# Performance work log

Measured on AMD Instinct MI355X. Metric: run time of the kernel, lower is better.

## Reference

```python
import jax, jax.numpy as jnp
import numpy as np

CONF_THRES = 0.25
IOU_THRES = 0.45
MAX_DET = 1000
MAX_WH = 4096.0  # class offset used by YOLOv5 for class-aware NMS
K = 1024         # fixed candidate count (static-shape stand-in for conf filtering)


def xywh2xyxy(b):
    cx, cy, w, h = b[..., 0], b[..., 1], b[..., 2], b[..., 3]
    return jnp.stack([cx - w / 2, cy - h / 2, cx + w / 2, cy + h / 2], axis=-1)


def pairwise_iou(boxes):
    # boxes: [K,4] xyxy -> [K,K] IoU
    x1, y1, x2, y2 = boxes[:, 0], boxes[:, 1], boxes[:, 2], boxes[:, 3]
    area = (x2 - x1) * (y2 - y1)
    ix1 = jnp.maximum(x1[:, None], x1[None, :])
    iy1 = jnp.maximum(y1[:, None], y1[None, :])
    ix2 = jnp.minimum(x2[:, None], x2[None, :])
    iy2 = jnp.minimum(y2[:, None], y2[None, :])
    inter = jnp.clip(ix2 - ix1, 0.0) * jnp.clip(iy2 - iy1, 0.0)
    return inter / (area[:, None] + area[None, :] - inter + 1e-9)


def nms_image(pred):
    # pred: [N, 5+nc] = xywh, obj, class scores
    boxes = xywh2xyxy(pred[:, :4])                 # [N,4]
    scores = pred[:, 5:] * pred[:, 4:5]            # conf = obj * cls
    conf = jnp.max(scores, axis=-1)                # [N]
    cls = jnp.argmax(scores, axis=-1)              # [N] int
    masked = jnp.where(conf > CONF_THRES, conf, -1.0)
    top_conf, idx = jax.lax.top_k(masked, K)       # sorted desc
    cand_boxes = boxes[idx]                        # [K,4]
    cand_cls = cls[idx]                            # [K]
    cand_valid = top_conf > 0.0                    # below-threshold slots are -1
    # class-aware NMS: offset boxes per class so different classes never overlap
    off_boxes = cand_boxes + (cand_cls.astype(pred.dtype) * MAX_WH)[:, None]
    iou = pairwise_iou(off_boxes)                  # [K,K]

    def step(suppressed, i):
        keep_i = jnp.logical_and(jnp.logical_not(suppressed[i]), cand_valid[i])
        suppressed = jnp.where(keep_i, jnp.logical_or(suppressed, iou[i] > IOU_THRES), suppressed)
        return suppressed, keep_i

    _, keep = jax.lax.scan(step, jnp.zeros((K,), dtype=bool), jnp.arange(K))
    sel_score = jnp.where(keep, top_conf, -1.0)
    fin_score, fin_idx = jax.lax.top_k(sel_score, MAX_DET)
    ok = fin_score > 0.0
    det = jnp.concatenate(
        [cand_boxes[fin_idx],
         top_conf[fin_idx][:, None],
         cand_cls[fin_idx].astype(pred.dtype)[:, None]],
        axis=-1,
    )  # [MAX_DET, 6] = x1,y1,x2,y2,conf,cls
    return jnp.where(ok[:, None], det, 0.0)


def setup_inputs() -> dict:
    key = jax.random.key(0)
    k1, k2, k3, k4 = jax.random.split(key, 4)
    B, N, NC = 16, 25200, 80
    cxcy = jax.random.uniform(k1, (B, N, 2), dtype=jnp.float32) * 640.0
    wh = jax.random.uniform(k2, (B, N, 2), dtype=jnp.float32) * 96.0 + 4.0
    obj = jax.random.uniform(k3, (B, N, 1), dtype=jnp.float32)
    cls = jax.random.uniform(k4, (B, N, NC), dtype=jnp.float32)
    pred = jnp.concatenate([cxcy, wh, obj, cls], axis=-1)
    return {"pred": pred}


def reference(pred):
    # [B, MAX_DET, 6] zero-padded detections per image
    return jax.vmap(nms_image)(pred)
```

## Files before the change

kernel.cpp:

```cpp
#include <hip/hip_runtime.h>
#include <stdint.h>

typedef unsigned int u32;
typedef unsigned long long u64;

#define BB 16
#define NN 25200
#define ROWLEN 85
#define KCAND 1024
#define MAXDET 1000
#define CONF_T 0.25f
#define IOU_T 0.45f
#define MAX_WH 4096.0f

__device__ __forceinline__ u32 f2key(float f) {
  u32 u = __float_as_uint(f);
  return (u & 0x80000000u) ? ~u : (u | 0x80000000u);
}
__device__ __forceinline__ float key2f(u32 k) {
  u32 u = (k & 0x80000000u) ? (k & 0x7FFFFFFFu) : ~k;
  return __uint_as_float(u);
}

__global__ __launch_bounds__(64) void k_score(const float* __restrict__ pred,
                                              float* __restrict__ masked,
                                              int* __restrict__ clsArr) {
  __shared__ float sh[64 * ROWLEN];
  const int t = threadIdx.x;
  const size_t blk = (size_t)blockIdx.x;
  const float4* src = (const float4*)(pred + blk * (64 * ROWLEN));
  float4* dst = (float4*)sh;
  #pragma unroll
  for (int i = 0; i < 21; ++i) dst[t + 64 * i] = src[t + 64 * i];
  if (t < 16) dst[t + 64 * 21] = src[t + 64 * 21];
  __syncthreads();
  const float* row = sh + t * ROWLEN;
  float obj = row[4];
  float v0 = -INFINITY, v1 = -INFINITY, v2 = -INFINITY, v3 = -INFINITY;
  int j0 = 0, j1 = 20, j2 = 40, j3 = 60;
  #pragma unroll
  for (int c = 0; c < 20; ++c) {
    float s0 = obj * row[5 + c];
    float s1 = obj * row[25 + c];
    float s2 = obj * row[45 + c];
    float s3 = obj * row[65 + c];
    if (s0 > v0) { v0 = s0; j0 = c; }
    if (s1 > v1) { v1 = s1; j1 = 20 + c; }
    if (s2 > v2) { v2 = s2; j2 = 40 + c; }
    if (s3 > v3) { v3 = s3; j3 = 60 + c; }
  }
  float v = v0; int j = j0;
  if (v1 > v) { v = v1; j = j1; }
  if (v2 > v) { v = v2; j = j2; }
  if (v3 > v) { v = v3; j = j3; }
  size_t r = blk * 64 + t;
  masked[r] = (v > CONF_T) ? v : -1.0f;
  clsArr[r] = j;
}

__device__ __forceinline__ void bt_apply(u64& e, u64 p, int m, int j, int k) {
  bool lower = ((m & j) == 0);
  bool dir = ((m & k) == 0);
  bool takeMax = (lower == dir);
  u64 mx = e > p ? e : p;
  u64 mn = e > p ? p : e;
  e = takeMax ? mx : mn;
}

__global__ __launch_bounds__(1024) void k_select(const float* __restrict__ pred,
                                                 const float* __restrict__ masked,
                                                 const int* __restrict__ clsArr,
                                                 float* __restrict__ candScore,
                                                 float* __restrict__ candBox,
                                                 int* __restrict__ candCls) {
  __shared__ u32 hist[16][257];
  __shared__ u64 buf[2048];
  __shared__ u32 sh_sel, sh_rem, sh_cnt;
  const int b = blockIdx.x;
  const int tid = threadIdx.x;
  const int lane = tid & 63;
  const int wv = tid >> 6;
  const float* m = masked + (size_t)b * NN;
  u32* histflat = (u32*)hist;

  u32 keys[25];
  #pragma unroll
  for (int it = 0; it < 25; ++it) {
    int n0 = tid + it * 1024;
    keys[it] = (n0 < NN) ? f2key(m[n0]) : 0u;
  }

  u32 prefix = 0, himask = 0, remaining = KCAND;
  for (int pass = 0; pass < 4; ++pass) {
    int shift = 24 - 8 * pass;
    for (int i = tid; i < 16 * 257; i += 1024) histflat[i] = 0;
    __syncthreads();
    #pragma unroll
    for (int it = 0; it < 25; ++it) {
      int n0 = tid + it * 1024;
      u32 key = keys[it];
      if (n0 < NN && (key & himask) == prefix)
        atomicAdd(&hist[wv][(key >> shift) & 255], 1u);
    }
    __syncthreads();
    if (wv == 0) {
      u32 c0 = 0, c1 = 0, c2 = 0, c3 = 0;
      #pragma unroll
      for (int w = 0; w < 16; ++w) {
        c0 += hist[w][4 * lane + 0];
        c1 += hist[w][4 * lane + 1];
        c2 += hist[w][4 * lane + 2];
        c3 += hist[w][4 * lane + 3];
      }
      u32 tl = c0 + c1 + c2 + c3;
      u32 incl = tl;
      #pragma unroll
      for (int off = 1; off <= 32; off <<= 1) {
        u32 o = __shfl_down(incl, off, 64);
        if (lane + off < 64) incl += o;
      }
      u32 S0 = incl;
      u32 S1 = S0 - c0;
      u32 S2 = S1 - c1;
      u32 S3 = S2 - c2;
      u32 S4 = S3 - c3;
      u32 rem = remaining;
      if (S0 >= rem && S1 < rem) { sh_sel = 4 * lane + 0; sh_rem = rem - S1; }
      if (S1 >= rem && S2 < rem) { sh_sel = 4 * lane + 1; sh_rem = rem - S2; }
      if (S2 >= rem && S3 < rem) { sh_sel = 4 * lane + 2; sh_rem = rem - S3; }
      if (S3 >= rem && S4 < rem) { sh_sel = 4 * lane + 3; sh_rem = rem - S4; }
    }
    __syncthreads();
    prefix |= (sh_sel << shift);
    remaining = sh_rem;
    himask |= (0xFFu << shift);
    __syncthreads();
  }
  const u32 T = prefix;
  if (tid == 0) sh_cnt = 0;
  __syncthreads();
  #pragma unroll
  for (int it = 0; it < 25; ++it) {
    int n0 = tid + it * 1024;
    u32 key = keys[it];
    bool match = (n0 < NN) && (key >= T);
    u64 bal = __ballot(match);
    if (bal) {
      int leader = __ffsll((unsigned long long)bal) - 1;
      u32 base = 0;
      u32 cnt = (u32)__popcll(bal);
      if (lane == leader) base = atomicAdd(&sh_cnt, cnt);
      base = __shfl(base, leader, 64);
      if (match) {
        u32 pos = base + (u32)__popcll(bal & ((1ull << lane) - 1ull));
        if (pos < 2048) buf[pos] = ((u64)key << 32) | (u32)(~(u32)n0);
      }
    }
  }
  __syncthreads();
  u32 c = sh_cnt; if (c > 2048) c = 2048;
  for (int t = tid; t < 2048; t += 1024) if (t >= (int)c) buf[t] = 0;
  __syncthreads();

  u64 e0 = buf[tid];
  u64 e1 = buf[tid + 1024];
  #pragma unroll
  for (int k = 2; k <= 64; k <<= 1) {
    #pragma unroll
    for (int j = k >> 1; j > 0; j >>= 1) {
      u64 p0 = __shfl_xor(e0, j, 64);
      u64 p1 = __shfl_xor(e1, j, 64);
      bt_apply(e0, p0, tid, j, k);
      bt_apply(e1, p1, tid + 1024, j, k);
    }
  }
  for (int k = 128; k <= 2048; k <<= 1) {
    int jstart = k >> 1;
    if (k == 2048) {
      u64 mx = e0 > e1 ? e0 : e1;
      u64 mn = e0 > e1 ? e1 : e0;
      e0 = mx; e1 = mn;
      jstart = 512;
    }
    for (int j = jstart; j >= 64; j >>= 1) {
      buf[tid] = e0; buf[tid + 1024] = e1;
      __syncthreads();
      u64 p0 = buf[tid ^ j];
      u64 p1 = buf[(tid ^ j) + 1024];
      bt_apply(e0, p0, tid, j, k);
      bt_apply(e1, p1, tid + 1024, j, k);
      __syncthreads();
    }
    #pragma unroll
    for (int j = 32; j > 0; j >>= 1) {
      u64 p0 = __shfl_xor(e0, j, 64);
      u64 p1 = __shfl_xor(e1, j, 64);
      bt_apply(e0, p0, tid, j, k);
      bt_apply(e1, p1, tid + 1024, j, k);
    }
  }
  {
    u64 e = e0;
    u32 key = (u32)(e >> 32);
    u32 idx = ~(u32)e;
    if (idx >= NN) idx = 0;
    float sc = key2f(key);
    size_t g = (size_t)b * KCAND + tid;
    candScore[g] = sc;
    const float* p = pred + ((size_t)b * NN + idx) * ROWLEN;
    float cx = p[0], cy = p[1], w = p[2], h = p[3];
    float4 bx;
    bx.x = cx - 0.5f * w;
    bx.y = cy - 0.5f * h;
    bx.z = cx + 0.5f * w;
    bx.w = cy + 0.5f * h;
    ((float4*)candBox)[g] = bx;
    candCls[g] = clsArr[(size_t)b * NN + idx];
  }
}

__global__ __launch_bounds__(256) void k_iou(const float* __restrict__ candBox,
                                             const int* __restrict__ candCls,
                                             u64* __restrict__ matT) {
  #pragma clang fp contract(off)
  __shared__ float sx1[KCAND], sy1[KCAND], sx2[KCAND], sy2[KCAND], sar[KCAND];
  const int b = blockIdx.y;
  const int r0 = blockIdx.x * 64;
  const int tid = threadIdx.x;
  for (int i = tid; i < KCAND; i += 256) {
    float4 bx = ((const float4*)candBox)[(size_t)b * KCAND + i];
    float off = (float)candCls[(size_t)b * KCAND + i] * MAX_WH;
    float x1 = bx.x + off, y1 = bx.y + off, x2 = bx.z + off, y2 = bx.w + off;
    sx1[i] = x1; sy1[i] = y1; sx2[i] = x2; sy2[i] = y2;
    sar[i] = (x2 - x1) * (y2 - y1);
  }
  __syncthreads();
  const int row = r0 + (tid & 63);
  const int wbase = tid >> 6;
  float rx1 = sx1[row], ry1 = sy1[row], rx2 = sx2[row], ry2 = sy2[row], rar = sar[row];
  for (int q = 0; q < 4; ++q) {
    int w = wbase + q * 4;
    int jb = w << 6;
    u64 mk = 0;
    for (int kk = 0; kk < 64; ++kk) {
      int jj = jb + kk;
      float ix1 = fmaxf(rx1, sx1[jj]);
      float iy1 = fmaxf(ry1, sy1[jj]);
      float ix2 = fminf(rx2, sx2[jj]);
      float iy2 = fminf(ry2, sy2[jj]);
      float dx = fmaxf(ix2 - ix1, 0.0f);
      float dy = fmaxf(iy2 - iy1, 0.0f);
      float inter = dx * dy;
      float den = rar + sar[jj];
      den = den - inter;
      den = den + 1e-9f;
      float iou = inter / den;
      if (iou > IOU_T) mk |= (1ull << kk);
    }
    matT[(((size_t)b * 16 + w) << 10) + row] = mk;
  }
}

__global__ __launch_bounds__(64, 1) void k_scan(const u64* __restrict__ matT,
                                                const float* __restrict__ candScore,
                                                u64* __restrict__ keepw) {
  const int b = blockIdx.x;
  const int lane = threadIdx.x;
  const u64* Mb = matT + ((size_t)b << 14);
  u64 vw[16];
  u64 dg16[16];
  #pragma unroll
  for (int w = 0; w < 16; ++w) {
    float sc = candScore[(size_t)b * KCAND + w * 64 + lane];
    vw[w] = __ballot(sc > 0.0f);
  }
  #pragma unroll
  for (int c = 0; c < 16; ++c)
    dg16[c] = Mb[((size_t)c << 10) + c * 64 + lane];

  u64 kcw[16];
  #pragma unroll
  for (int c = 0; c < 16; ++c) {
    u64 acc = 0;
    #pragma unroll
    for (int cp = 0; cp < c; ++cp) {
      u64 wv = Mb[((size_t)c << 10) + cp * 64 + lane];
      if ((kcw[cp] >> lane) & 1ull) acc |= wv;
    }
    #pragma unroll
    for (int st = 1; st < 64; st <<= 1) acc |= __shfl_xor(acc, st, 64);
    u64 d = dg16[c];
    u64 s = acc;
    u64 kc = 0;
    u64 vc = vw[c];
    #pragma unroll
    for (int g = 0; g < 8; ++g) {
      u64 dgp[8];
      #pragma unroll
      for (int j = 0; j < 8; ++j) dgp[j] = __shfl(d, g * 8 + j, 64);
      #pragma unroll
      for (int j = 0; j < 8; ++j) {
        int i = g * 8 + j;
        bool ok = !((s >> i) & 1ull) && ((vc >> i) & 1ull);
        if (ok) { s |= dgp[j]; kc |= (1ull << i); }
      }
    }
    kcw[c] = kc;
  }
  if (lane < 16) keepw[(size_t)b * 16 + lane] = kcw[lane];
}

__global__ __launch_bounds__(1024) void k_out(const u64* __restrict__ keepw,
                                              const float* __restrict__ candScore,
                                              const float* __restrict__ candBox,
                                              const int* __restrict__ candCls,
                                              float* __restrict__ out) {
  __shared__ u64 kw[16];
  const int b = blockIdx.x;
  const int tid = threadIdx.x;
  if (tid < 16) kw[tid] = keepw[(size_t)b * 16 + tid];
  __syncthreads();
  int total = 0;
  #pragma unroll
  for (int w = 0; w < 16; ++w) total += __popcll(kw[w]);
  int kept_eff = total < MAXDET ? total : MAXDET;
  const int t = tid;
  u64 word = kw[t >> 6];
  int bit = (int)((word >> (t & 63)) & 1ull);
  int rank = 0;
  for (int w = 0; w < (t >> 6); ++w) rank += __popcll(kw[w]);
  rank += __popcll(word & ((1ull << (t & 63)) - 1ull));
  float* outb = out + (size_t)b * MAXDET * 6;
  if (bit && rank < MAXDET) {
    size_t g = (size_t)b * KCAND + t;
    float4 bx = ((const float4*)candBox)[g];
    float sc = candScore[g];
    float cf = (float)candCls[g];
    float* o = outb + (size_t)rank * 6;
    o[0] = bx.x; o[1] = bx.y; o[2] = bx.z; o[3] = bx.w; o[4] = sc; o[5] = cf;
  }
  if (t < MAXDET && t >= kept_eff) {
    float* o = outb + (size_t)t * 6;
    o[0] = 0.f; o[1] = 0.f; o[2] = 0.f; o[3] = 0.f; o[4] = 0.f; o[5] = 0.f;
  }
}

extern "C" void kernel_launch(void* const* d_in, const int* in_sizes, int n_in,
                              void* d_out, int out_size, void* d_ws, size_t ws_size,
                              hipStream_t stream) {
  const float* pred = (const float*)d_in[0];
  float* out = (float*)d_out;
  char* ws = (char*)d_ws;
  size_t o = 0;
  float* masked    = (float*)(ws + o); o += (size_t)BB * NN * 4;
  int*   clsArr    = (int*)  (ws + o); o += (size_t)BB * NN * 4;
  float* candScore = (float*)(ws + o); o += (size_t)BB * KCAND * 4;
  float* candBox   = (float*)(ws + o); o += (size_t)BB * KCAND * 16;
  int*   candCls   = (int*)  (ws + o); o += (size_t)BB * KCAND * 4;
  o = (o + 255) & ~(size_t)255;
  u64*   matT      = (u64*)  (ws + o); o += (size_t)BB * KCAND * 16 * 8;
  u64*   keepw     = (u64*)  (ws + o); o += (size_t)BB * 16 * 8;

  const int rows = BB * NN;
  k_score<<<rows / 64, 64, 0, stream>>>(pred, masked, clsArr);
  k_select<<<BB, 1024, 0, stream>>>(pred, masked, clsArr, candScore, candBox, candCls);
  k_iou<<<dim3(16, BB), 256, 0, stream>>>(candBox, candCls, matT);
  k_scan<<<BB, 64, 0, stream>>>(matT, candScore, keepw);
  k_out<<<BB, 1024, 0, stream>>>(keepw, candScore, candBox, candCls, out);
}
```

Measured before the change: 340.9 us.

## Fuse NMS scan and output kernels, staging mask matrix in LDS

Merges the single-wave suppression scan with the output compaction kernel, so one launch and the global keep-word round trip go away. The lower-triangular part of the mask matrix (column blocks 0..14) is loaded cooperatively into shared memory by all 1024 threads before the scan. The last block's 15 words are preloaded into registers. The serial scan then reads from LDS instead of global memory. The cost is about 60KB of LDS per block, plus 960 threads idling during the serial scan.

Result: slower. 358.3 us (+5.1%).

```diff
diff --git a/kernel.cpp b/kernel.cpp
--- a/kernel.cpp
+++ b/kernel.cpp
@@ -261,74 +261,97 @@
   }
 }
 
-__global__ __launch_bounds__(64, 1) void k_scan(const u64* __restrict__ matT,
-                                                const float* __restrict__ candScore,
-                                                u64* __restrict__ keepw) {
-  const int b = blockIdx.x;
-  const int lane = threadIdx.x;
-  const u64* Mb = matT + ((size_t)b << 14);
-  u64 vw[16];
-  u64 dg16[16];
-  #pragma unroll
-  for (int w = 0; w < 16; ++w) {
-    float sc = candScore[(size_t)b * KCAND + w * 64 + lane];
-    vw[w] = __ballot(sc > 0.0f);
-  }
-  #pragma unroll
-  for (int c = 0; c < 16; ++c)
-    dg16[c] = Mb[((size_t)c << 10) + c * 64 + lane];
-
-  u64 kcw[16];
-  #pragma unroll
-  for (int c = 0; c < 16; ++c) {
-    u64 acc = 0;
-    #pragma unroll
-    for (int cp = 0; cp < c; ++cp) {
-      u64 wv = Mb[((size_t)c << 10) + cp * 64 + lane];
-      if ((kcw[cp] >> lane) & 1ull) acc |= wv;
-    }
-    #pragma unroll
-    for (int st = 1; st < 64; st <<= 1) acc |= __shfl_xor(acc, st, 64);
-    u64 d = dg16[c];
-    u64 s = acc;
-    u64 kc = 0;
-    u64 vc = vw[c];
-    #pragma unroll
-    for (int g = 0; g < 8; ++g) {
-      u64 dgp[8];
-      #pragma unroll
-      for (int j = 0; j < 8; ++j) dgp[j] = __shfl(d, g * 8 + j, 64);
-      #pragma unroll
-      for (int j = 0; j < 8; ++j) {
-        int i = g * 8 + j;
-        bool ok = !((s >> i) & 1ull) && ((vc >> i) & 1ull);
-        if (ok) { s |= dgp[j]; kc |= (1ull << i); }
-      }
-    }
-    kcw[c] = kc;
-  }
-  if (lane < 16) keepw[(size_t)b * 16 + lane] = kcw[lane];
-}
-
-__global__ __launch_bounds__(1024) void k_out(const u64* __restrict__ keepw,
-                                              const float* __restrict__ candScore,
-                                              const float* __restrict__ candBox,
-                                              const int* __restrict__ candCls,
-                                              float* __restrict__ out) {
-  __shared__ u64 kw[16];
+__global__ __launch_bounds__(1024) void k_scan_out(const u64* __restrict__ matT,
+                                                   const float* __restrict__ candScore,
+                                                   const float* __restrict__ candBox,
+                                                   const int* __restrict__ candCls,
+                                                   float* __restrict__ out) {
+  __shared__ u64 sm[7680];
+  __shared__ u64 sKeep[16];
   const int b = blockIdx.x;
   const int tid = threadIdx.x;
-  if (tid < 16) kw[tid] = keepw[(size_t)b * 16 + tid];
-  __syncthreads();
+  const u64* Mb = matT + ((size_t)b << 14);
+
+  u64 vw[16], dg16[16], pre15[15];
+  if (tid < 64) {
+    const int lane = tid;
+    #pragma unroll
+    for (int w = 0; w < 16; ++w) {
+      float sc = candScore[(size_t)b * KCAND + w * 64 + lane];
+      vw[w] = __ballot(sc > 0.0f);
+    }
+    #pragma unroll
+    for (int c = 0; c < 16; ++c)
+      dg16[c] = Mb[((size_t)c << 10) + c * 64 + lane];
+    #pragma unroll
+    for (int cp = 0; cp < 15; ++cp)
+      pre15[cp] = Mb[((size_t)15 << 10) + cp * 64 + lane];
+  }
+
+  {
+    int base = 0;
+    #pragma unroll
+    for (int c = 0; c < 15; ++c) {
+      int L = (c + 1) << 6;
+      for (int i = tid; i < L; i += 1024) sm[base + i] = Mb[((size_t)c << 10) + i];
+      base += L;
+    }
+  }
+  __syncthreads();
+
+  if (tid < 64) {
+    const int lane = tid;
+    u64 kcw[16];
+    int cbase = 0;
+    #pragma unroll
+    for (int c = 0; c < 16; ++c) {
+      u64 acc = 0;
+      if (c < 15) {
+        #pragma unroll
+        for (int cp = 0; cp < c; ++cp) {
+          u64 wv2 = sm[cbase + cp * 64 + lane];
+          if ((kcw[cp] >> lane) & 1ull) acc |= wv2;
+        }
+      } else {
+        #pragma unroll
+        for (int cp = 0; cp < 15; ++cp) {
+          if ((kcw[cp] >> lane) & 1ull) acc |= pre15[cp];
+        }
+      }
+      #pragma unroll
+      for (int st = 1; st < 64; st <<= 1) acc |= __shfl_xor(acc, st, 64);
+      u64 d = dg16[c];
+      u64 s = acc;
+      u64 kc = 0;
+      u64 vc = vw[c];
+      #pragma unroll
+      for (int g = 0; g < 8; ++g) {
+        u64 dgp[8];
+        #pragma unroll
+        for (int j = 0; j < 8; ++j) dgp[j] = __shfl(d, g * 8 + j, 64);
+        #pragma unroll
+        for (int j = 0; j < 8; ++j) {
+          int i = g * 8 + j;
+          bool ok = !((s >> i) & 1ull) && ((vc >> i) & 1ull);
+          if (ok) { s |= dgp[j]; kc |= (1ull << i); }
+        }
+      }
+      kcw[c] = kc;
+      if (c < 15) cbase += (c + 1) << 6;
+    }
+    if (lane < 16) sKeep[lane] = kcw[lane];
+  }
+  __syncthreads();
+
   int total = 0;
   #pragma unroll
-  for (int w = 0; w < 16; ++w) total += __popcll(kw[w]);
+  for (int w = 0; w < 16; ++w) total += __popcll(sKeep[w]);
   int kept_eff = total < MAXDET ? total : MAXDET;
   const int t = tid;
-  u64 word = kw[t >> 6];
+  u64 word = sKeep[t >> 6];
   int bit = (int)((word >> (t & 63)) & 1ull);
   int rank = 0;
-  for (int w = 0; w < (t >> 6); ++w) rank += __popcll(kw[w]);
+  for (int w = 0; w < (t >> 6); ++w) rank += __popcll(sKeep[w]);
   rank += __popcll(word & ((1ull << (t & 63)) - 1ull));
   float* outb = out + (size_t)b * MAXDET * 6;
   if (bit && rank < MAXDET) {
@@ -359,12 +382,10 @@
   int*   candCls   = (int*)  (ws + o); o += (size_t)BB * KCAND * 4;
   o = (o + 255) & ~(size_t)255;
   u64*   matT      = (u64*)  (ws + o); o += (size_t)BB * KCAND * 16 * 8;
-  u64*   keepw     = (u64*)  (ws + o); o += (size_t)BB * 16 * 8;
 
   const int rows = BB * NN;
   k_score<<<rows / 64, 64, 0, stream>>>(pred, masked, clsArr);
   k_select<<<BB, 1024, 0, stream>>>(pred, masked, clsArr, candScore, candBox, candCls);
   k_iou<<<dim3(16, BB), 256, 0, stream>>>(candBox, candCls, matT);
-  k_scan<<<BB, 64, 0, stream>>>(matT, candScore, keepw);
-  k_out<<<BB, 1024, 0, stream>>>(keepw, candScore, candBox, candCls, out);
-}
+  k_scan_out<<<BB, 1024, 0, stream>>>(matT, candScore, candBox, candCls, out);
+}
```
